# Kernel tuning notes

Hardware: AMD Instinct MI355X
Metric: run time of the kernel (lower is better)

Reference implementation:

```python
import jax, jax.numpy as jnp
import numpy as np

DT = 0.1  # module buffer `dt`
I_DIM, H_DIM, BATCH, SEQ = 128, 64, 8, 4096


def setup_inputs() -> dict:
    key = jax.random.key(0)
    ks = jax.random.split(key, 6)
    return {
        "x": jax.random.normal(ks[0], (BATCH, SEQ, I_DIM), dtype=jnp.float32),
        "B": jax.random.uniform(ks[1], (I_DIM, H_DIM), dtype=jnp.float32),
        "C_tilde": jax.random.uniform(ks[2], (I_DIM, H_DIM), dtype=jnp.float32),
        "Lambda": jax.random.uniform(ks[3], (I_DIM, 1, H_DIM), dtype=jnp.float32),
        "P": jax.random.uniform(ks[4], (I_DIM, H_DIM), dtype=jnp.float32),
        "Q": jax.random.uniform(ks[5], (I_DIM, H_DIM), dtype=jnp.float32),
    }


def _compute_K(B, C_tilde, Lambda, P, Q, L):
    # omega_k = exp(2*pi*i*k/L), k = 0..L-1
    n = jnp.arange(L, dtype=jnp.float32)
    omega = jnp.exp((2j * jnp.pi / L) * n).astype(jnp.complex64)          # [L]
    g = (2.0 / DT) * ((1.0 - omega) / (1.0 + omega))                      # [L]
    # denominator: [I, L, H] complex (the big intermediate)
    inv = 1.0 / (g[None, :, None] - Lambda.astype(jnp.complex64))
    a0, a1 = jnp.conj(C_tilde), Q                                          # [I, H]
    b0, b1 = B, P                                                          # [I, H]
    # Cauchy dot products: sum over hidden dim -> [I, L]
    k00 = jnp.einsum('ih,ilh->il', (a0 * b0).astype(jnp.complex64), inv)
    k01 = jnp.einsum('ih,ilh->il', (a0 * b1).astype(jnp.complex64), inv)
    k10 = jnp.einsum('ih,ilh->il', (a1 * b0).astype(jnp.complex64), inv)
    k11 = jnp.einsum('ih,ilh->il', (a1 * b1).astype(jnp.complex64), inv)
    c = 2.0 / (1.0 + omega)                                                # [L]
    K_hat = c[None, :] * (k00 - k01 * (1.0 + k11) * k10)                   # [I, L]
    # irfft crops input along last axis to L//2 + 1 bins (matches torch)
    return jnp.fft.irfft(K_hat, n=L, axis=-1)                              # [I, L] real


def reference(x, B, C_tilde, Lambda, P, Q):
    Bz, L, I = x.shape
    K = _compute_K(B, C_tilde, Lambda, P, Q, L)        # [I, L]
    xt = jnp.transpose(x, (0, 2, 1))                   # [B, I, L]
    n2 = 2 * L
    x_fft = jnp.fft.rfft(xt, n=n2, axis=2)             # zero-pad to 2L -> [B, I, L+1]
    K_fft = jnp.fft.rfft(K, n=n2, axis=1)[None]        # [1, I, L+1]
    y = jnp.fft.irfft(x_fft * K_fft, n=n2, axis=2)[:, :, :L]
    return jnp.transpose(y, (0, 2, 1))                 # [B, L, I]
```

## Files before the change

kernel.cpp:

```cpp
#include <hip/hip_runtime.h>

#define I_DIM 128
#define H_DIM 64
#define BATCH 8
#define SEQ   4096
#define NBIN  (SEQ/2 + 1)
#define NBIN2 (SEQ + 1)

#define SZ(a) ((a) ^ (((a) >> 4) & 15) ^ (((a) >> 8) & 15))

__device__ float  g_xT[(size_t)BATCH * I_DIM * SEQ];
__device__ float2 g_Hh[I_DIM * NBIN];
__device__ float2 g_Kf[I_DIM * NBIN2];
__device__ float2 g_Xf[(size_t)BATCH * I_DIM * SEQ];
__device__ float  g_Yt[(size_t)BATCH * I_DIM * SEQ];

__device__ inline float2 cmul(float2 a, float2 b) {
    return make_float2(a.x * b.x - a.y * b.y, a.x * b.y + a.y * b.x);
}
__device__ inline float2 cadd(float2 a, float2 b) { return make_float2(a.x + b.x, a.y + b.y); }
__device__ inline float2 csub(float2 a, float2 b) { return make_float2(a.x - b.x, a.y - b.y); }

__device__ inline void dft8(float2 a[8]) {
    const float C = 0.70710678118654752f;
    float2 s0 = cadd(a[0], a[4]), s1 = cadd(a[1], a[5]);
    float2 s2 = cadd(a[2], a[6]), s3 = cadd(a[3], a[7]);
    float2 d0 = csub(a[0], a[4]), d1 = csub(a[1], a[5]);
    float2 d2 = csub(a[2], a[6]), d3 = csub(a[3], a[7]);
    d1 = make_float2(C * (d1.x + d1.y), C * (d1.y - d1.x));
    d2 = make_float2(d2.y, -d2.x);
    d3 = make_float2(C * (d3.y - d3.x), -C * (d3.x + d3.y));
    {
        float2 p0 = cadd(s0, s2), p1 = cadd(s1, s3);
        float2 m0 = csub(s0, s2), m1 = csub(s1, s3);
        m1 = make_float2(m1.y, -m1.x);
        a[0] = cadd(p0, p1); a[4] = csub(p0, p1);
        a[2] = cadd(m0, m1); a[6] = csub(m0, m1);
    }
    {
        float2 p0 = cadd(d0, d2), p1 = cadd(d1, d3);
        float2 m0 = csub(d0, d2), m1 = csub(d1, d3);
        m1 = make_float2(m1.y, -m1.x);
        a[1] = cadd(p0, p1); a[5] = csub(p0, p1);
        a[3] = cadd(m0, m1); a[7] = csub(m0, m1);
    }
}

__device__ inline void dft8hz(float2 x0, float2 x1, float2 x2, float2 x3,
                              float2 b[8]) {
    const float C = 0.70710678118654752f;
    float2 p0 = cadd(x0, x2), p1 = cadd(x1, x3);
    float2 m0 = csub(x0, x2), m1t = csub(x1, x3);
    float2 m1 = make_float2(m1t.y, -m1t.x);
    b[0] = cadd(p0, p1); b[4] = csub(p0, p1);
    b[2] = cadd(m0, m1); b[6] = csub(m0, m1);
    float2 c1 = make_float2(C * (x1.x + x1.y), C * (x1.y - x1.x));
    float2 c2 = make_float2(x2.y, -x2.x);
    float2 c3 = make_float2(C * (x3.y - x3.x), -C * (x3.x + x3.y));
    float2 q0 = cadd(x0, c2), q1 = cadd(c1, c3);
    float2 n0 = csub(x0, c2), n1t = csub(c1, c3);
    float2 n1 = make_float2(n1t.y, -n1t.x);
    b[1] = cadd(q0, q1); b[5] = csub(q0, q1);
    b[3] = cadd(n0, n1); b[7] = csub(n0, n1);
}

__device__ inline void combine16(const float2 e[8], const float2 o[8],
                                 float2 b[16]) {
    const float C  = 0.70710678118654752f;
    const float C1 = 0.92387953251128674f;
    const float S1 = 0.38268343236508977f;
    float2 t;
    b[0] = cadd(e[0], o[0]);  b[8]  = csub(e[0], o[0]);
    t = cmul(o[1], make_float2( C1, -S1)); b[1] = cadd(e[1], t); b[9]  = csub(e[1], t);
    t = cmul(o[2], make_float2(  C,  -C)); b[2] = cadd(e[2], t); b[10] = csub(e[2], t);
    t = cmul(o[3], make_float2( S1, -C1)); b[3] = cadd(e[3], t); b[11] = csub(e[3], t);
    t = make_float2(o[4].y, -o[4].x);      b[4] = cadd(e[4], t); b[12] = csub(e[4], t);
    t = cmul(o[5], make_float2(-S1, -C1)); b[5] = cadd(e[5], t); b[13] = csub(e[5], t);
    t = cmul(o[6], make_float2( -C,  -C)); b[6] = cadd(e[6], t); b[14] = csub(e[6], t);
    t = cmul(o[7], make_float2(-C1, -S1)); b[7] = cadd(e[7], t); b[15] = csub(e[7], t);
}

__device__ inline void dft16(float2 a[16]) {
    float2 e[8] = {a[0], a[2], a[4], a[6], a[8], a[10], a[12], a[14]};
    float2 o[8] = {a[1], a[3], a[5], a[7], a[9], a[11], a[13], a[15]};
    dft8(e); dft8(o);
    combine16(e, o, a);
}

__device__ inline void s1_twiddle_write(float2* __restrict__ lds, int u,
                                        float2 b[16]) {
    float sn, cs;
    __sincosf((float)(-6.283185307179586 / 4096.0) * (float)u, &sn, &cs);
    float2 w1 = make_float2(cs, sn);
    float2 w2 = cmul(w1, w1), w3 = cmul(w2, w1), w4 = cmul(w2, w2);
    float2 w5 = cmul(w3, w2), w6 = cmul(w3, w3), w7 = cmul(w4, w3);
    float2 w8 = cmul(w4, w4);
    const int base = 16 * u;
    lds[SZ(base + 0)]  = b[0];
    lds[SZ(base + 1)]  = cmul(b[1], w1);
    lds[SZ(base + 2)]  = cmul(b[2], w2);
    lds[SZ(base + 3)]  = cmul(b[3], w3);
    lds[SZ(base + 4)]  = cmul(b[4], w4);
    lds[SZ(base + 5)]  = cmul(b[5], w5);
    lds[SZ(base + 6)]  = cmul(b[6], w6);
    lds[SZ(base + 7)]  = cmul(b[7], w7);
    lds[SZ(base + 8)]  = cmul(b[8], w8);
    lds[SZ(base + 9)]  = cmul(cmul(b[9],  w1), w8);
    lds[SZ(base + 10)] = cmul(cmul(b[10], w2), w8);
    lds[SZ(base + 11)] = cmul(cmul(b[11], w3), w8);
    lds[SZ(base + 12)] = cmul(cmul(b[12], w4), w8);
    lds[SZ(base + 13)] = cmul(cmul(b[13], w5), w8);
    lds[SZ(base + 14)] = cmul(cmul(b[14], w6), w8);
    lds[SZ(base + 15)] = cmul(cmul(b[15], w7), w8);
}

template <int S>
__device__ inline void stage16(float2* __restrict__ lds, int u) {
    float2 d[16];
#pragma unroll
    for (int j = 0; j < 16; ++j) d[j] = lds[SZ(u + 256 * j)];
    __syncthreads();
    const int q = u & (S - 1);
    dft16(d);
    if constexpr (S < 256) {
        float sn, cs;
        __sincosf((float)(-6.283185307179586 / 4096.0) * (float)(u - q), &sn, &cs);
        float2 w1 = make_float2(cs, sn);
        float2 w2 = cmul(w1, w1), w3 = cmul(w2, w1), w4 = cmul(w2, w2);
        float2 w5 = cmul(w3, w2), w6 = cmul(w3, w3), w7 = cmul(w4, w3);
        float2 w8 = cmul(w4, w4);
        d[1]  = cmul(d[1], w1);  d[2]  = cmul(d[2], w2);
        d[3]  = cmul(d[3], w3);  d[4]  = cmul(d[4], w4);
        d[5]  = cmul(d[5], w5);  d[6]  = cmul(d[6], w6);
        d[7]  = cmul(d[7], w7);  d[8]  = cmul(d[8], w8);
        d[9]  = cmul(cmul(d[9],  w1), w8);
        d[10] = cmul(cmul(d[10], w2), w8);
        d[11] = cmul(cmul(d[11], w3), w8);
        d[12] = cmul(cmul(d[12], w4), w8);
        d[13] = cmul(cmul(d[13], w5), w8);
        d[14] = cmul(cmul(d[14], w6), w8);
        d[15] = cmul(cmul(d[15], w7), w8);
    }
    const int base = 16 * u - 15 * q;
#pragma unroll
    for (int k = 0; k < 16; ++k)
        lds[SZ(base + k * S)] = d[k];
    __syncthreads();
}

__device__ inline float2 khat_bin(int i, int k,
                                  const float* __restrict__ Bm,
                                  const float* __restrict__ Cm,
                                  const float* __restrict__ Lm,
                                  const float* __restrict__ Pm,
                                  const float* __restrict__ Qm) {
    float theta = (float)(6.283185307179586 / (double)SEQ) * (float)k;
    float sn, cs;
    sincosf(theta, &sn, &cs);
    float tr = 1.0f - cs, ti = -sn;
    float br = 1.0f + cs, bi = sn;
    float idn = 1.0f / (br * br + bi * bi);
    float gr = 20.0f * (tr * br + ti * bi) * idn;
    float gi = 20.0f * (ti * br - tr * bi) * idn;
    float cr = 2.0f * br * idn;
    float ci = -2.0f * bi * idn;

    const float* Brow = Bm + i * H_DIM;
    const float* Crow = Cm + i * H_DIM;
    const float* Lrow = Lm + i * H_DIM;
    const float* Prow = Pm + i * H_DIM;
    const float* Qrow = Qm + i * H_DIM;

    float k00r = 0.f, k00i = 0.f, k01r = 0.f, k01i = 0.f;
    float k10r = 0.f, k10i = 0.f, k11r = 0.f, k11i = 0.f;
#pragma unroll 8
    for (int h = 0; h < H_DIM; ++h) {
        float lam = Lrow[h];
        float drr = gr - lam;
        float dii = gi;
        float im = 1.0f / (drr * drr + dii * dii);
        float ivr = drr * im;
        float ivi = -dii * im;
        float bv = Brow[h], cv = Crow[h], pv = Prow[h], qv = Qrow[h];
        float cb = cv * bv;
        float cp = cv * pv;
        float qb = qv * bv;
        float qp = qv * pv;
        k00r += cb * ivr; k00i += cb * ivi;
        k01r += cp * ivr; k01i += cp * ivi;
        k10r += qb * ivr; k10i += qb * ivi;
        k11r += qp * ivr; k11i += qp * ivi;
    }
    float t1r = 1.0f + k11r, t1i = k11i;
    float t2r = k01r * t1r - k01i * t1i;
    float t2i = k01r * t1i + k01i * t1r;
    float t3r = t2r * k10r - t2i * k10i;
    float t3i = t2r * k10i + t2i * k10r;
    float nr = k00r - t3r, ni = k00i - t3i;
    return make_float2(cr * nr - ci * ni, cr * ni + ci * nr);
}

__global__ __launch_bounds__(256) void k1_transpose_khat(const float* __restrict__ x,
                                                         const float* __restrict__ Bm,
                                                         const float* __restrict__ Cm,
                                                         const float* __restrict__ Lm,
                                                         const float* __restrict__ Pm,
                                                         const float* __restrict__ Qm) {
    __shared__ float t[64][65];
    const int blk = blockIdx.x;
    const int b = blk >> 7;
    const int rest = blk & 127;
    const int nt = rest >> 1;
    const int it = rest & 1;
    const int tx = threadIdx.x & 63;
    const int ty = threadIdx.x >> 6;
    const int n0 = nt * 64, i0 = it * 64;

    const float* xb = x + (size_t)b * SEQ * I_DIM;
#pragma unroll
    for (int r = 0; r < 16; ++r) {
        int nl = r * 4 + ty;
        t[nl][tx] = xb[(size_t)(n0 + nl) * I_DIM + i0 + tx];
    }
    __syncthreads();
#pragma unroll
    for (int r = 0; r < 16; ++r) {
        int il = r * 4 + ty;
        g_xT[((size_t)b * I_DIM + i0 + il) * SEQ + n0 + tx] = t[tx][il];
    }

    const int ch = blk >> 3, sl = blk & 7;
    const int k = sl * 256 + threadIdx.x;
    g_Hh[(size_t)ch * NBIN + k] = khat_bin(ch, k, Bm, Cm, Lm, Pm, Qm);
    if (sl == 0 && threadIdx.x == 0)
        g_Hh[(size_t)ch * NBIN + 2048] = khat_bin(ch, 2048, Bm, Cm, Lm, Pm, Qm);
}

__global__ __launch_bounds__(256) void k2_kprep_fwd() {
    __shared__ float2 L[4096];
    const int u = threadIdx.x;

    if (blockIdx.x < I_DIM) {
        const int i = blockIdx.x;
        const float2* Hrow = g_Hh + (size_t)i * NBIN;

        {
            float2 d[16];
#pragma unroll
            for (int j = 0; j < 16; ++j) {
                int m = u + (j << 8);
                float2 h;
                if (m <= 2048) h = Hrow[m];
                else { float2 tt = Hrow[4096 - m]; h = make_float2(tt.x, -tt.y); }
                d[j] = make_float2(h.x, -h.y);
            }
            dft16(d);
            s1_twiddle_write(L, u, d);
            __syncthreads();
        }
        stage16<16>(L, u);
        stage16<256>(L, u);

        {
            const float2 W32[16] = {
                make_float2( 1.00000000f,  0.00000000f), make_float2( 0.98078528f, -0.19509032f),
                make_float2( 0.92387953f, -0.38268343f), make_float2( 0.83146961f, -0.55557023f),
                make_float2( 0.70710678f, -0.70710678f), make_float2( 0.55557023f, -0.83146961f),
                make_float2( 0.38268343f, -0.92387953f), make_float2( 0.19509032f, -0.98078528f),
                make_float2( 0.00000000f, -1.00000000f), make_float2(-0.19509032f, -0.98078528f),
                make_float2(-0.38268343f, -0.92387953f), make_float2(-0.55557023f, -0.83146961f),
                make_float2(-0.70710678f, -0.70710678f), make_float2(-0.83146961f, -0.55557023f),
                make_float2(-0.92387953f, -0.38268343f), make_float2(-0.98078528f, -0.19509032f)};
            float snu, csu;
            __sincosf((float)(-3.141592653589793 / 4096.0) * (float)u, &snu, &csu);
            float2 wu = make_float2(csu, snu);
            float2 v[16];
#pragma unroll
            for (int j = 0; j < 16; ++j) {
                float kr = L[SZ(u + (j << 8))].x * (1.0f / 4096.0f);
                float2 w = cmul(wu, W32[j]);
                v[j] = make_float2(kr * w.x, kr * w.y);
            }
            __syncthreads();
            dft16(v);
            s1_twiddle_write(L, u, v);
            __syncthreads();
        }
        stage16<16>(L, u);

        float2 e[16];
#pragma unroll
        for (int j = 0; j < 16; ++j) e[j] = L[SZ(u + (j << 8))];
        dft16(e);
        float2* Kfrow = g_Kf + (size_t)i * NBIN2;
#pragma unroll
        for (int k = 0; k < 8; ++k)
            Kfrow[2 * (u + (k << 8)) + 1] = e[k];
        for (int r = u; r <= 2048; r += 256)
            Kfrow[2 * r] = Hrow[r];
    } else {
        const int blk = blockIdx.x - I_DIM;
        const int b = blk & 7;
        const int i = blk >> 3;
        const float2* xrow = (const float2*)(g_xT + ((size_t)b * I_DIM + i) * SEQ);

        float2 xx[8];
#pragma unroll
        for (int j = 0; j < 8; ++j) xx[j] = xrow[u + (j << 8)];
        float2 e[8], o[8], bb[16];
        dft8hz(xx[0], xx[2], xx[4], xx[6], e);
        dft8hz(xx[1], xx[3], xx[5], xx[7], o);
        combine16(e, o, bb);
        s1_twiddle_write(L, u, bb);
        __syncthreads();

        stage16<16>(L, u);

        float2 f[16];
#pragma unroll
        for (int j = 0; j < 16; ++j) f[j] = L[SZ(u + (j << 8))];
        dft16(f);
        float2* dst = g_Xf + (size_t)blk * SEQ;
#pragma unroll
        for (int k = 0; k < 16; ++k)
            dst[u + (k << 8)] = f[k];
    }
}

__global__ __launch_bounds__(256) void k3_combine_inv() {
    __shared__ float2 L[4096];
    const int u = threadIdx.x;
    const int blk = blockIdx.x;
    const int b = blk & 7;
    const int i = blk >> 3;
    const float2* Xf = g_Xf + (size_t)blk * SEQ;
    const float2* Kfrow = g_Kf + (size_t)i * NBIN2;

    float2 d[16];
#pragma unroll
    for (int j = 0; j < 16; ++j) {
        int m = u + (j << 8);
        int mm = (4096 - m) & 4095;
        float2 Zq = Xf[m];
        float2 Zr = Xf[mm];
        float2 Km  = Kfrow[m];
        float2 Km2 = Kfrow[4096 - m];
        float sn, cs;
        __sincosf((float)(-3.141592653589793 / 4096.0) * (float)m, &sn, &cs);
        float pr = Zq.x + Zr.x, pi2 = Zq.y - Zr.y;
        float dr = Zq.x - Zr.x, di = Zq.y + Zr.y;
        float jt_r = -sn * dr - cs * di;
        float jt_i =  cs * dr - sn * di;
        float2 Xm  = make_float2(0.5f * (pr - jt_r),  0.5f * ( pi2 - jt_i));
        float2 Xm2 = make_float2(0.5f * (pr + jt_r),  0.5f * (-pi2 - jt_i));
        float2 Ym  = cmul(Xm,  Km);
        float2 Ym2 = cmul(Xm2, Km2);
        float qr = Ym.x + Ym2.x, qi = Ym.y - Ym2.y;
        float er = Ym.x - Ym2.x, ei = Ym.y + Ym2.y;
        float gr2 = sn * er - cs * ei;
        float gi2 = sn * ei + cs * er;
        d[j] = make_float2(0.5f * (qr + gr2), -0.5f * (qi + gi2));
    }
    dft16(d);
    s1_twiddle_write(L, u, d);
    __syncthreads();

    stage16<16>(L, u);

    float2 e[16];
#pragma unroll
    for (int j = 0; j < 16; ++j) e[j] = L[SZ(u + (j << 8))];
    dft16(e);
    const float inv = 1.0f / 4096.0f;
    float2* yrow = (float2*)(g_Yt + ((size_t)b * I_DIM + i) * SEQ);
#pragma unroll
    for (int k = 0; k < 8; ++k)
        yrow[u + (k << 8)] = make_float2(e[k].x * inv, -e[k].y * inv);
}

__global__ __launch_bounds__(256) void k4_transpose_out(float* __restrict__ y) {
    __shared__ float t[64][65];
    const int blk = blockIdx.x;
    const int b = blk >> 7;
    const int rest = blk & 127;
    const int nt = rest >> 1;
    const int it = rest & 1;
    const int tx = threadIdx.x & 63;
    const int ty = threadIdx.x >> 6;
    const int n0 = nt * 64, i0 = it * 64;

#pragma unroll
    for (int r = 0; r < 16; ++r) {
        int il = r * 4 + ty;
        t[il][tx] = g_Yt[((size_t)b * I_DIM + i0 + il) * SEQ + n0 + tx];
    }
    __syncthreads();
    float* yb = y + (size_t)b * SEQ * I_DIM;
#pragma unroll
    for (int r = 0; r < 16; ++r) {
        int nl = r * 4 + ty;
        yb[(size_t)(n0 + nl) * I_DIM + i0 + tx] = t[tx][nl];
    }
}

extern "C" void kernel_launch(void* const* d_in, const int* in_sizes, int n_in,
                              void* d_out, int out_size, void* d_ws, size_t ws_size,
                              hipStream_t stream) {
    const float* x  = (const float*)d_in[0];
    const float* Bm = (const float*)d_in[1];
    const float* Cm = (const float*)d_in[2];
    const float* Lm = (const float*)d_in[3];
    const float* Pm = (const float*)d_in[4];
    const float* Qm = (const float*)d_in[5];
    float* out = (float*)d_out;

    k1_transpose_khat<<<1024, 256, 0, stream>>>(x, Bm, Cm, Lm, Pm, Qm);
    k2_kprep_fwd<<<I_DIM + BATCH * I_DIM, 256, 0, stream>>>();
    k3_combine_inv<<<BATCH * I_DIM, 256, 0, stream>>>();
    k4_transpose_out<<<1024, 256, 0, stream>>>(out);
}
```

Before: 71.68 us.

## Fuse four kernels into one persistent cooperative kernel with grid syncs

Replaces the four separate launches with a single cooperative persistent kernel that loops over work units and uses grid-wide barriers between the transpose/Khat, FFT prep, combine/inverse, and output transpose phases. The grid size comes from an occupancy query and is capped at 768 blocks. Plain multi-kernel launches remain as a fallback. The aim is to remove inter-kernel launch gaps and drain/fill tails. The cost is grid.sync overhead, a per-call occupancy query on the host, and extra __syncthreads calls to reuse shared memory across loop iterations. The kprep phase also runs on only 128 blocks while the rest handle the forward FFTs, which can leave the load uneven.

```diff
diff --git a/kernel.cpp b/kernel.cpp
--- a/kernel.cpp
+++ b/kernel.cpp
@@ -1,4 +1,7 @@
 #include <hip/hip_runtime.h>
+#include <hip/hip_cooperative_groups.h>
+
+namespace cg = cooperative_groups;
 
 #define I_DIM 128
 #define H_DIM 64
@@ -200,22 +203,22 @@
     return make_float2(cr * nr - ci * ni, cr * ni + ci * nr);
 }
 
-__global__ __launch_bounds__(256) void k1_transpose_khat(const float* __restrict__ x,
-                                                         const float* __restrict__ Bm,
-                                                         const float* __restrict__ Cm,
-                                                         const float* __restrict__ Lm,
-                                                         const float* __restrict__ Pm,
-                                                         const float* __restrict__ Qm) {
-    __shared__ float t[64][65];
-    const int blk = blockIdx.x;
-    const int b = blk >> 7;
-    const int rest = blk & 127;
+__device__ inline void p1_unit(float2* __restrict__ L, int tid, int w,
+                               const float* __restrict__ x,
+                               const float* __restrict__ Bm,
+                               const float* __restrict__ Cm,
+                               const float* __restrict__ Lm,
+                               const float* __restrict__ Pm,
+                               const float* __restrict__ Qm) {
+    float (*t)[65] = reinterpret_cast<float(*)[65]>(L);
+    const int b = w >> 7;
+    const int rest = w & 127;
     const int nt = rest >> 1;
     const int it = rest & 1;
-    const int tx = threadIdx.x & 63;
-    const int ty = threadIdx.x >> 6;
+    const int tx = tid & 63;
+    const int ty = tid >> 6;
     const int n0 = nt * 64, i0 = it * 64;
-
+    __syncthreads();
     const float* xb = x + (size_t)b * SEQ * I_DIM;
 #pragma unroll
     for (int r = 0; r < 16; ++r) {
@@ -228,114 +231,100 @@
         int il = r * 4 + ty;
         g_xT[((size_t)b * I_DIM + i0 + il) * SEQ + n0 + tx] = t[tx][il];
     }
-
-    const int ch = blk >> 3, sl = blk & 7;
-    const int k = sl * 256 + threadIdx.x;
+    const int ch = w >> 3, sl = w & 7;
+    const int k = sl * 256 + tid;
     g_Hh[(size_t)ch * NBIN + k] = khat_bin(ch, k, Bm, Cm, Lm, Pm, Qm);
-    if (sl == 0 && threadIdx.x == 0)
+    if (sl == 0 && tid == 0)
         g_Hh[(size_t)ch * NBIN + 2048] = khat_bin(ch, 2048, Bm, Cm, Lm, Pm, Qm);
 }
 
-__global__ __launch_bounds__(256) void k2_kprep_fwd() {
-    __shared__ float2 L[4096];
-    const int u = threadIdx.x;
-
-    if (blockIdx.x < I_DIM) {
-        const int i = blockIdx.x;
-        const float2* Hrow = g_Hh + (size_t)i * NBIN;
-
-        {
-            float2 d[16];
-#pragma unroll
-            for (int j = 0; j < 16; ++j) {
-                int m = u + (j << 8);
-                float2 h;
-                if (m <= 2048) h = Hrow[m];
-                else { float2 tt = Hrow[4096 - m]; h = make_float2(tt.x, -tt.y); }
-                d[j] = make_float2(h.x, -h.y);
-            }
-            dft16(d);
-            s1_twiddle_write(L, u, d);
-            __syncthreads();
+__device__ inline void kprep_unit(float2* __restrict__ L, int u, int i) {
+    const float2* Hrow = g_Hh + (size_t)i * NBIN;
+    {
+        float2 d[16];
+#pragma unroll
+        for (int j = 0; j < 16; ++j) {
+            int m = u + (j << 8);
+            float2 h;
+            if (m <= 2048) h = Hrow[m];
+            else { float2 tt = Hrow[4096 - m]; h = make_float2(tt.x, -tt.y); }
+            d[j] = make_float2(h.x, -h.y);
         }
-        stage16<16>(L, u);
-        stage16<256>(L, u);
-
-        {
-            const float2 W32[16] = {
-                make_float2( 1.00000000f,  0.00000000f), make_float2( 0.98078528f, -0.19509032f),
-                make_float2( 0.92387953f, -0.38268343f), make_float2( 0.83146961f, -0.55557023f),
-                make_float2( 0.70710678f, -0.70710678f), make_float2( 0.55557023f, -0.83146961f),
-                make_float2( 0.38268343f, -0.92387953f), make_float2( 0.19509032f, -0.98078528f),
-                make_float2( 0.00000000f, -1.00000000f), make_float2(-0.19509032f, -0.98078528f),
-                make_float2(-0.38268343f, -0.92387953f), make_float2(-0.55557023f, -0.83146961f),
-                make_float2(-0.70710678f, -0.70710678f), make_float2(-0.83146961f, -0.55557023f),
-                make_float2(-0.92387953f, -0.38268343f), make_float2(-0.98078528f, -0.19509032f)};
-            float snu, csu;
-            __sincosf((float)(-3.141592653589793 / 4096.0) * (float)u, &snu, &csu);
-            float2 wu = make_float2(csu, snu);
-            float2 v[16];
-#pragma unroll
-            for (int j = 0; j < 16; ++j) {
-                float kr = L[SZ(u + (j << 8))].x * (1.0f / 4096.0f);
-                float2 w = cmul(wu, W32[j]);
-                v[j] = make_float2(kr * w.x, kr * w.y);
-            }
-            __syncthreads();
-            dft16(v);
-            s1_twiddle_write(L, u, v);
-            __syncthreads();
+        dft16(d);
+        __syncthreads();
+        s1_twiddle_write(L, u, d);
+        __syncthreads();
+    }
+    stage16<16>(L, u);
+    stage16<256>(L, u);
+    {
+        const float2 W32[16] = {
+            make_float2( 1.00000000f,  0.00000000f), make_float2( 0.98078528f, -0.19509032f),
+            make_float2( 0.92387953f, -0.38268343f), make_float2( 0.83146961f, -0.55557023f),
+            make_float2( 0.70710678f, -0.70710678f), make_float2( 0.55557023f, -0.83146961f),
+            make_float2( 0.38268343f, -0.92387953f), make_float2( 0.19509032f, -0.98078528f),
+            make_float2( 0.00000000f, -1.00000000f), make_float2(-0.19509032f, -0.98078528f),
+            make_float2(-0.38268343f, -0.92387953f), make_float2(-0.55557023f, -0.83146961f),
+            make_float2(-0.70710678f, -0.70710678f), make_float2(-0.83146961f, -0.55557023f),
+            make_float2(-0.92387953f, -0.38268343f), make_float2(-0.98078528f, -0.19509032f)};
+        float snu, csu;
+        __sincosf((float)(-3.141592653589793 / 4096.0) * (float)u, &snu, &csu);
+        float2 wu = make_float2(csu, snu);
+        float2 v[16];
+#pragma unroll
+        for (int j = 0; j < 16; ++j) {
+            float kr = L[SZ(u + (j << 8))].x * (1.0f / 4096.0f);
+            float2 w = cmul(wu, W32[j]);
+            v[j] = make_float2(kr * w.x, kr * w.y);
         }
-        stage16<16>(L, u);
-
-        float2 e[16];
-#pragma unroll
-        for (int j = 0; j < 16; ++j) e[j] = L[SZ(u + (j << 8))];
-        dft16(e);
-        float2* Kfrow = g_Kf + (size_t)i * NBIN2;
-#pragma unroll
-        for (int k = 0; k < 8; ++k)
-            Kfrow[2 * (u + (k << 8)) + 1] = e[k];
-        for (int r = u; r <= 2048; r += 256)
-            Kfrow[2 * r] = Hrow[r];
-    } else {
-        const int blk = blockIdx.x - I_DIM;
-        const int b = blk & 7;
-        const int i = blk >> 3;
-        const float2* xrow = (const float2*)(g_xT + ((size_t)b * I_DIM + i) * SEQ);
-
-        float2 xx[8];
-#pragma unroll
-        for (int j = 0; j < 8; ++j) xx[j] = xrow[u + (j << 8)];
-        float2 e[8], o[8], bb[16];
-        dft8hz(xx[0], xx[2], xx[4], xx[6], e);
-        dft8hz(xx[1], xx[3], xx[5], xx[7], o);
-        combine16(e, o, bb);
-        s1_twiddle_write(L, u, bb);
         __syncthreads();
-
-        stage16<16>(L, u);
-
-        float2 f[16];
-#pragma unroll
-        for (int j = 0; j < 16; ++j) f[j] = L[SZ(u + (j << 8))];
-        dft16(f);
-        float2* dst = g_Xf + (size_t)blk * SEQ;
-#pragma unroll
-        for (int k = 0; k < 16; ++k)
-            dst[u + (k << 8)] = f[k];
-    }
-}
-
-__global__ __launch_bounds__(256) void k3_combine_inv() {
-    __shared__ float2 L[4096];
-    const int u = threadIdx.x;
-    const int blk = blockIdx.x;
-    const int b = blk & 7;
-    const int i = blk >> 3;
-    const float2* Xf = g_Xf + (size_t)blk * SEQ;
+        dft16(v);
+        s1_twiddle_write(L, u, v);
+        __syncthreads();
+    }
+    stage16<16>(L, u);
+    float2 e[16];
+#pragma unroll
+    for (int j = 0; j < 16; ++j) e[j] = L[SZ(u + (j << 8))];
+    dft16(e);
+    float2* Kfrow = g_Kf + (size_t)i * NBIN2;
+#pragma unroll
+    for (int k = 0; k < 8; ++k)
+        Kfrow[2 * (u + (k << 8)) + 1] = e[k];
+    for (int r = u; r <= 2048; r += 256)
+        Kfrow[2 * r] = Hrow[r];
+}
+
+__device__ inline void fwd_row(float2* __restrict__ L, int u, int row) {
+    const int b = row & 7;
+    const int i = row >> 3;
+    const float2* xrow = (const float2*)(g_xT + ((size_t)b * I_DIM + i) * SEQ);
+    float2 xx[8];
+#pragma unroll
+    for (int j = 0; j < 8; ++j) xx[j] = xrow[u + (j << 8)];
+    float2 e[8], o[8], bb[16];
+    dft8hz(xx[0], xx[2], xx[4], xx[6], e);
+    dft8hz(xx[1], xx[3], xx[5], xx[7], o);
+    combine16(e, o, bb);
+    __syncthreads();
+    s1_twiddle_write(L, u, bb);
+    __syncthreads();
+    stage16<16>(L, u);
+    float2 f[16];
+#pragma unroll
+    for (int j = 0; j < 16; ++j) f[j] = L[SZ(u + (j << 8))];
+    dft16(f);
+    float2* dst = g_Xf + (size_t)row * SEQ;
+#pragma unroll
+    for (int k = 0; k < 16; ++k)
+        dst[u + (k << 8)] = f[k];
+}
+
+__device__ inline void combine_row(float2* __restrict__ L, int u, int row) {
+    const int b = row & 7;
+    const int i = row >> 3;
+    const float2* Xf = g_Xf + (size_t)row * SEQ;
     const float2* Kfrow = g_Kf + (size_t)i * NBIN2;
-
     float2 d[16];
 #pragma unroll
     for (int j = 0; j < 16; ++j) {
@@ -362,11 +351,10 @@
         d[j] = make_float2(0.5f * (qr + gr2), -0.5f * (qi + gi2));
     }
     dft16(d);
+    __syncthreads();
     s1_twiddle_write(L, u, d);
     __syncthreads();
-
     stage16<16>(L, u);
-
     float2 e[16];
 #pragma unroll
     for (int j = 0; j < 16; ++j) e[j] = L[SZ(u + (j << 8))];
@@ -378,17 +366,17 @@
         yrow[u + (k << 8)] = make_float2(e[k].x * inv, -e[k].y * inv);
 }
 
-__global__ __launch_bounds__(256) void k4_transpose_out(float* __restrict__ y) {
-    __shared__ float t[64][65];
-    const int blk = blockIdx.x;
-    const int b = blk >> 7;
-    const int rest = blk & 127;
+__device__ inline void p4_unit(float2* __restrict__ L, int tid, int w,
+                               float* __restrict__ y) {
+    float (*t)[65] = reinterpret_cast<float(*)[65]>(L);
+    const int b = w >> 7;
+    const int rest = w & 127;
     const int nt = rest >> 1;
     const int it = rest & 1;
-    const int tx = threadIdx.x & 63;
-    const int ty = threadIdx.x >> 6;
+    const int tx = tid & 63;
+    const int ty = tid >> 6;
     const int n0 = nt * 64, i0 = it * 64;
-
+    __syncthreads();
 #pragma unroll
     for (int r = 0; r < 16; ++r) {
         int il = r * 4 + ty;
@@ -401,6 +389,65 @@
         int nl = r * 4 + ty;
         yb[(size_t)(n0 + nl) * I_DIM + i0 + tx] = t[tx][nl];
     }
+}
+
+__global__ __launch_bounds__(256, 3) void s4_mega(const float* __restrict__ x,
+                                                  const float* __restrict__ Bm,
+                                                  const float* __restrict__ Cm,
+                                                  const float* __restrict__ Lm,
+                                                  const float* __restrict__ Pm,
+                                                  const float* __restrict__ Qm,
+                                                  float* __restrict__ y) {
+    cg::grid_group grid = cg::this_grid();
+    __shared__ float2 L[4096];
+    const int tid = threadIdx.x;
+    const int bid = blockIdx.x;
+    const int G = gridDim.x;
+
+    for (int w = bid; w < 1024; w += G)
+        p1_unit(L, tid, w, x, Bm, Cm, Lm, Pm, Qm);
+    grid.sync();
+
+    if (bid < I_DIM) {
+        kprep_unit(L, tid, bid);
+    } else {
+        for (int w = bid - I_DIM; w < 1024; w += G - I_DIM)
+            fwd_row(L, tid, w);
+    }
+    grid.sync();
+
+    for (int w = bid; w < 1024; w += G)
+        combine_row(L, tid, w);
+    grid.sync();
+
+    for (int w = bid; w < 1024; w += G)
+        p4_unit(L, tid, w, y);
+}
+
+__global__ __launch_bounds__(256) void fb_k1(const float* __restrict__ x,
+                                             const float* __restrict__ Bm,
+                                             const float* __restrict__ Cm,
+                                             const float* __restrict__ Lm,
+                                             const float* __restrict__ Pm,
+                                             const float* __restrict__ Qm) {
+    __shared__ float2 L[4096];
+    p1_unit(L, threadIdx.x, blockIdx.x, x, Bm, Cm, Lm, Pm, Qm);
+}
+
+__global__ __launch_bounds__(256) void fb_k2() {
+    __shared__ float2 L[4096];
+    if (blockIdx.x < I_DIM) kprep_unit(L, threadIdx.x, blockIdx.x);
+    else                    fwd_row(L, threadIdx.x, blockIdx.x - I_DIM);
+}
+
+__global__ __launch_bounds__(256) void fb_k3() {
+    __shared__ float2 L[4096];
+    combine_row(L, threadIdx.x, blockIdx.x);
+}
+
+__global__ __launch_bounds__(256) void fb_k4(float* __restrict__ y) {
+    __shared__ float2 L[4096];
+    p4_unit(L, threadIdx.x, blockIdx.x, y);
 }
 
 extern "C" void kernel_launch(void* const* d_in, const int* in_sizes, int n_in,
@@ -414,8 +461,25 @@
     const float* Qm = (const float*)d_in[5];
     float* out = (float*)d_out;
 
-    k1_transpose_khat<<<1024, 256, 0, stream>>>(x, Bm, Cm, Lm, Pm, Qm);
-    k2_kprep_fwd<<<I_DIM + BATCH * I_DIM, 256, 0, stream>>>();
-    k3_combine_inv<<<BATCH * I_DIM, 256, 0, stream>>>();
-    k4_transpose_out<<<1024, 256, 0, stream>>>(out);
-}
+    int blocksPerCU = 0;
+    hipError_t qerr = hipOccupancyMaxActiveBlocksPerMultiprocessor(
+        &blocksPerCU, (const void*)s4_mega, 256, 0);
+    bool launched = false;
+    if (qerr == hipSuccess && blocksPerCU > 0) {
+        int G = blocksPerCU * 256;
+        if (G > 768) G = 768;
+        if (G >= 192) {
+            void* args[7] = { (void*)&x, (void*)&Bm, (void*)&Cm, (void*)&Lm,
+                              (void*)&Pm, (void*)&Qm, (void*)&out };
+            hipError_t lerr = hipLaunchCooperativeKernel(
+                (const void*)s4_mega, dim3(G), dim3(256), args, 0, stream);
+            launched = (lerr == hipSuccess);
+        }
+    }
+    if (!launched) {
+        fb_k1<<<1024, 256, 0, stream>>>(x, Bm, Cm, Lm, Pm, Qm);
+        fb_k2<<<I_DIM + BATCH * I_DIM, 256, 0, stream>>>();
+        fb_k3<<<BATCH * I_DIM, 256, 0, stream>>>();
+        fb_k4<<<1024, 256, 0, stream>>>(out);
+    }
+}
```

Measured after the change: 94.04 us. +31.2%, slower.

## Fuse forward FFT of x into the spectral multiply and inverse FFT kernel

Applied to the files above, without the earlier changes.

The forward FFT of each x row is moved out of the combined K-prep kernel and into the combine/inverse kernel. The spectrum stays in shared memory instead of going through the global g_Xf buffer, which removes a full write and read of that intermediate. K preparation now runs as its own 128-block kernel. The trade-off is that the 128 K-prep blocks no longer overlap with the x FFT work, and the fused kernel does a longer sequential chain per block with an extra barrier.

```diff
diff --git a/kernel.cpp b/kernel.cpp
--- a/kernel.cpp
+++ b/kernel.cpp
@@ -12,7 +12,6 @@
 __device__ float  g_xT[(size_t)BATCH * I_DIM * SEQ];
 __device__ float2 g_Hh[I_DIM * NBIN];
 __device__ float2 g_Kf[I_DIM * NBIN2];
-__device__ float2 g_Xf[(size_t)BATCH * I_DIM * SEQ];
 __device__ float  g_Yt[(size_t)BATCH * I_DIM * SEQ];
 
 __device__ inline float2 cmul(float2 a, float2 b) {
@@ -236,113 +235,98 @@
         g_Hh[(size_t)ch * NBIN + 2048] = khat_bin(ch, 2048, Bm, Cm, Lm, Pm, Qm);
 }
 
-__global__ __launch_bounds__(256) void k2_kprep_fwd() {
+__global__ __launch_bounds__(256) void k2_kprep() {
     __shared__ float2 L[4096];
     const int u = threadIdx.x;
-
-    if (blockIdx.x < I_DIM) {
-        const int i = blockIdx.x;
-        const float2* Hrow = g_Hh + (size_t)i * NBIN;
-
-        {
-            float2 d[16];
-#pragma unroll
-            for (int j = 0; j < 16; ++j) {
-                int m = u + (j << 8);
-                float2 h;
-                if (m <= 2048) h = Hrow[m];
-                else { float2 tt = Hrow[4096 - m]; h = make_float2(tt.x, -tt.y); }
-                d[j] = make_float2(h.x, -h.y);
-            }
-            dft16(d);
-            s1_twiddle_write(L, u, d);
-            __syncthreads();
+    const int i = blockIdx.x;
+    const float2* Hrow = g_Hh + (size_t)i * NBIN;
+
+    {
+        float2 d[16];
+#pragma unroll
+        for (int j = 0; j < 16; ++j) {
+            int m = u + (j << 8);
+            float2 h;
+            if (m <= 2048) h = Hrow[m];
+            else { float2 tt = Hrow[4096 - m]; h = make_float2(tt.x, -tt.y); }
+            d[j] = make_float2(h.x, -h.y);
         }
-        stage16<16>(L, u);
-        stage16<256>(L, u);
-
-        {
-            const float2 W32[16] = {
-                make_float2( 1.00000000f,  0.00000000f), make_float2( 0.98078528f, -0.19509032f),
-                make_float2( 0.92387953f, -0.38268343f), make_float2( 0.83146961f, -0.55557023f),
-                make_float2( 0.70710678f, -0.70710678f), make_float2( 0.55557023f, -0.83146961f),
-                make_float2( 0.38268343f, -0.92387953f), make_float2( 0.19509032f, -0.98078528f),
-                make_float2( 0.00000000f, -1.00000000f), make_float2(-0.19509032f, -0.98078528f),
-                make_float2(-0.38268343f, -0.92387953f), make_float2(-0.55557023f, -0.83146961f),
-                make_float2(-0.70710678f, -0.70710678f), make_float2(-0.83146961f, -0.55557023f),
-                make_float2(-0.92387953f, -0.38268343f), make_float2(-0.98078528f, -0.19509032f)};
-            float snu, csu;
-            __sincosf((float)(-3.141592653589793 / 4096.0) * (float)u, &snu, &csu);
-            float2 wu = make_float2(csu, snu);
-            float2 v[16];
-#pragma unroll
-            for (int j = 0; j < 16; ++j) {
-                float kr = L[SZ(u + (j << 8))].x * (1.0f / 4096.0f);
-                float2 w = cmul(wu, W32[j]);
-                v[j] = make_float2(kr * w.x, kr * w.y);
-            }
-            __syncthreads();
-            dft16(v);
-            s1_twiddle_write(L, u, v);
-            __syncthreads();
+        dft16(d);
+        s1_twiddle_write(L, u, d);
+        __syncthreads();
+    }
+    stage16<16>(L, u);
+    stage16<256>(L, u);
+
+    {
+        const float2 W32[16] = {
+            make_float2( 1.00000000f,  0.00000000f), make_float2( 0.98078528f, -0.19509032f),
+            make_float2( 0.92387953f, -0.38268343f), make_float2( 0.83146961f, -0.55557023f),
+            make_float2( 0.70710678f, -0.70710678f), make_float2( 0.55557023f, -0.83146961f),
+            make_float2( 0.38268343f, -0.92387953f), make_float2( 0.19509032f, -0.98078528f),
+            make_float2( 0.00000000f, -1.00000000f), make_float2(-0.19509032f, -0.98078528f),
+            make_float2(-0.38268343f, -0.92387953f), make_float2(-0.55557023f, -0.83146961f),
+            make_float2(-0.70710678f, -0.70710678f), make_float2(-0.83146961f, -0.55557023f),
+            make_float2(-0.92387953f, -0.38268343f), make_float2(-0.98078528f, -0.19509032f)};
+        float snu, csu;
+        __sincosf((float)(-3.141592653589793 / 4096.0) * (float)u, &snu, &csu);
+        float2 wu = make_float2(csu, snu);
+        float2 v[16];
+#pragma unroll
+        for (int j = 0; j < 16; ++j) {
+            float kr = L[SZ(u + (j << 8))].x * (1.0f / 4096.0f);
+            float2 w = cmul(wu, W32[j]);
+            v[j] = make_float2(kr * w.x, kr * w.y);
         }
-        stage16<16>(L, u);
-
-        float2 e[16];
-#pragma unroll
-        for (int j = 0; j < 16; ++j) e[j] = L[SZ(u + (j << 8))];
-        dft16(e);
-        float2* Kfrow = g_Kf + (size_t)i * NBIN2;
-#pragma unroll
-        for (int k = 0; k < 8; ++k)
-            Kfrow[2 * (u + (k << 8)) + 1] = e[k];
-        for (int r = u; r <= 2048; r += 256)
-            Kfrow[2 * r] = Hrow[r];
-    } else {
-        const int blk = blockIdx.x - I_DIM;
-        const int b = blk & 7;
-        const int i = blk >> 3;
-        const float2* xrow = (const float2*)(g_xT + ((size_t)b * I_DIM + i) * SEQ);
-
-        float2 xx[8];
-#pragma unroll
-        for (int j = 0; j < 8; ++j) xx[j] = xrow[u + (j << 8)];
+        __syncthreads();
+        dft16(v);
+        s1_twiddle_write(L, u, v);
+        __syncthreads();
+    }
+    stage16<16>(L, u);
+
+    float2 e[16];
+#pragma unroll
+    for (int j = 0; j < 16; ++j) e[j] = L[SZ(u + (j << 8))];
+    dft16(e);
+    float2* Kfrow = g_Kf + (size_t)i * NBIN2;
+#pragma unroll
+    for (int k = 0; k < 8; ++k)
+        Kfrow[2 * (u + (k << 8)) + 1] = e[k];
+    for (int r = u; r <= 2048; r += 256)
+        Kfrow[2 * r] = Hrow[r];
+}
+
+__global__ __launch_bounds__(256) void k3_fused_conv() {
+    __shared__ float2 L[4096];
+    const int u = threadIdx.x;
+    const int blk = blockIdx.x;
+    const int b = blk & 7;
+    const int i = blk >> 3;
+
+    const float2* xrow = (const float2*)(g_xT + ((size_t)b * I_DIM + i) * SEQ);
+    float2 xx[8];
+#pragma unroll
+    for (int j = 0; j < 8; ++j) xx[j] = xrow[u + (j << 8)];
+    {
         float2 e[8], o[8], bb[16];
         dft8hz(xx[0], xx[2], xx[4], xx[6], e);
         dft8hz(xx[1], xx[3], xx[5], xx[7], o);
         combine16(e, o, bb);
         s1_twiddle_write(L, u, bb);
         __syncthreads();
-
-        stage16<16>(L, u);
-
-        float2 f[16];
-#pragma unroll
-        for (int j = 0; j < 16; ++j) f[j] = L[SZ(u + (j << 8))];
-        dft16(f);
-        float2* dst = g_Xf + (size_t)blk * SEQ;
-#pragma unroll
-        for (int k = 0; k < 16; ++k)
-            dst[u + (k << 8)] = f[k];
-    }
-}
-
-__global__ __launch_bounds__(256) void k3_combine_inv() {
-    __shared__ float2 L[4096];
-    const int u = threadIdx.x;
-    const int blk = blockIdx.x;
-    const int b = blk & 7;
-    const int i = blk >> 3;
-    const float2* Xf = g_Xf + (size_t)blk * SEQ;
+    }
+    stage16<16>(L, u);
+    stage16<256>(L, u);
+
     const float2* Kfrow = g_Kf + (size_t)i * NBIN2;
-
     float2 d[16];
 #pragma unroll
     for (int j = 0; j < 16; ++j) {
         int m = u + (j << 8);
         int mm = (4096 - m) & 4095;
-        float2 Zq = Xf[m];
-        float2 Zr = Xf[mm];
+        float2 Zq = L[SZ(m)];
+        float2 Zr = L[SZ(mm)];
         float2 Km  = Kfrow[m];
         float2 Km2 = Kfrow[4096 - m];
         float sn, cs;
@@ -361,21 +345,22 @@
         float gi2 = sn * ei + cs * er;
         d[j] = make_float2(0.5f * (qr + gr2), -0.5f * (qi + gi2));
     }
+    __syncthreads();
+
     dft16(d);
     s1_twiddle_write(L, u, d);
     __syncthreads();
-
     stage16<16>(L, u);
 
-    float2 e[16];
-#pragma unroll
-    for (int j = 0; j < 16; ++j) e[j] = L[SZ(u + (j << 8))];
-    dft16(e);
+    float2 f[16];
+#pragma unroll
+    for (int j = 0; j < 16; ++j) f[j] = L[SZ(u + (j << 8))];
+    dft16(f);
     const float inv = 1.0f / 4096.0f;
     float2* yrow = (float2*)(g_Yt + ((size_t)b * I_DIM + i) * SEQ);
 #pragma unroll
     for (int k = 0; k < 8; ++k)
-        yrow[u + (k << 8)] = make_float2(e[k].x * inv, -e[k].y * inv);
+        yrow[u + (k << 8)] = make_float2(f[k].x * inv, -f[k].y * inv);
 }
 
 __global__ __launch_bounds__(256) void k4_transpose_out(float* __restrict__ y) {
@@ -415,7 +400,7 @@
     float* out = (float*)d_out;
 
     k1_transpose_khat<<<1024, 256, 0, stream>>>(x, Bm, Cm, Lm, Pm, Qm);
-    k2_kprep_fwd<<<I_DIM + BATCH * I_DIM, 256, 0, stream>>>();
-    k3_combine_inv<<<BATCH * I_DIM, 256, 0, stream>>>();
+    k2_kprep<<<I_DIM, 256, 0, stream>>>();
+    k3_fused_conv<<<BATCH * I_DIM, 256, 0, stream>>>();
     k4_transpose_out<<<1024, 256, 0, stream>>>(out);
 }
```

Result: slower. 80.19 us (+11.9%).
